# Performance work log

Measured on AMD Instinct MI355X. Metric: run time of the kernel, lower is better.

The kernel has to match this reference:

```python
import jax, jax.numpy as jnp
import numpy as np

B, T, C, H, DH, L, V = 16, 1023, 384, 6, 64, 6, 256
FF = 4 * C
EPS = 1e-5


def _ln(x, g, b):
    mu = x.mean(-1, keepdims=True)
    var = ((x - mu) ** 2).mean(-1, keepdims=True)
    return (x - mu) * jax.lax.rsqrt(var + EPS) * g + b


def setup_inputs() -> dict:
    key = jax.random.key(0)
    ks = jax.random.split(key, 12)
    n = lambda k, shp: jax.random.normal(k, shp, dtype=jnp.float32) * 0.02
    return {
        "x": jax.random.randint(ks[0], (B, T), 0, V),
        "targets": jax.random.randint(ks[1], (B, T), 0, V),
        "tok_emb": n(ks[2], (V, C)),
        "pos_emb": n(ks[3], (T, C)),
        "Wq": n(ks[4], (L, C, C)), "Wk": n(ks[5], (L, C, C)), "Wv": n(ks[6], (L, C, C)),
        "Wo": n(ks[7], (L, C, C)), "bo": jnp.zeros((L, C)),
        "ln1_g": jnp.ones((L, C)), "ln1_b": jnp.zeros((L, C)),
        "ln2_g": jnp.ones((L, C)), "ln2_b": jnp.zeros((L, C)),
        "W1": n(ks[8], (L, C, FF)), "b1": jnp.zeros((L, FF)),
        "W2": n(ks[9], (L, FF, C)), "b2": jnp.zeros((L, C)),
        "lnf_g": jnp.ones((C,)), "lnf_b": jnp.zeros((C,)),
        "Wf": n(ks[10], (C, V)), "bf": jnp.zeros((V,)),
    }


def _forward(x, targets, tok_emb, pos_emb, Wq, Wk, Wv, Wo, bo,
             ln1_g, ln1_b, ln2_g, ln2_b, W1, b1, W2, b2, lnf_g, lnf_b, Wf, bf):
    h = tok_emb[x] + pos_emb[None, :, :]  # [B,T,C]
    tril = jnp.tril(jnp.ones((T, T), bool))

    def heads(z, W):  # [B,T,C] @ [C,C] -> [B,H,T,DH]
        return jnp.einsum('btc,cd->btd', z, W).reshape(B, T, H, DH).transpose(0, 2, 1, 3)

    def layer(h, p):
        wq, wk, wv, wo, bo_, g1, be1, g2, be2, w1, bb1, w2, bb2 = p
        z = _ln(h, g1, be1)
        q, k, v = heads(z, wq), heads(z, wk), heads(z, wv)
        qk = jnp.einsum('bhtd,bhsd->bhts', q, k) * (DH ** -0.5)
        zm = jnp.where(tril, qk, 0.0)
        # faithful to torch: masked_fill_(zeromask == 0, -inf)
        zm = jnp.where(zm == 0.0, -jnp.inf, zm)
        att = jax.nn.softmax(zm, axis=-1)  # dropout = identity (eval)
        o = jnp.einsum('bhts,bhsd->bhtd', att, v).transpose(0, 2, 1, 3).reshape(B, T, C)
        h = h + jnp.einsum('btc,cd->btd', o, wo) + bo_
        z2 = _ln(h, g2, be2)
        ff = jax.nn.relu(jnp.einsum('btc,cf->btf', z2, w1) + bb1)
        h = h + jnp.einsum('btf,fc->btc', ff, w2) + bb2
        return h, None

    params = (Wq, Wk, Wv, Wo, bo, ln1_g, ln1_b, ln2_g, ln2_b, W1, b1, W2, b2)
    h, _ = jax.lax.scan(layer, h, params)
    logits = jnp.einsum('btc,cv->btv', _ln(h, lnf_g, lnf_b), Wf) + bf
    logits2 = logits.reshape(B * T, V)
    logp = jax.nn.log_softmax(logits2, axis=-1)
    loss = -jnp.take_along_axis(logp, targets.reshape(B * T, 1), axis=1).mean()
    return logits2, loss


def reference(x, targets, tok_emb, pos_emb, Wq, Wk, Wv, Wo, bo,
              ln1_g, ln1_b, ln2_g, ln2_b, W1, b1, W2, b2, lnf_g, lnf_b, Wf, bf):
    return _forward(x, targets, tok_emb, pos_emb, Wq, Wk, Wv, Wo, bo,
                    ln1_g, ln1_b, ln2_g, ln2_b, W1, b1, W2, b2, lnf_g, lnf_b, Wf, bf)
```

## Files before the change

kernel.cpp:

```cpp
#include <hip/hip_runtime.h>
#include <hip/hip_bf16.h>
#include <math.h>

#define B_  16
#define T_  1023
#define C_  384
#define H_  6
#define DH_ 64
#define L_  6
#define V_  256
#define FF_ 1536
#define M_  (B_*T_)
#define MP_ 16384
#define EPS_ 1e-5f

typedef __attribute__((ext_vector_type(8))) short bf16x8;
typedef __attribute__((ext_vector_type(4))) short short4v;
typedef __attribute__((ext_vector_type(4))) float f32x4;

__device__ inline short f2bf(float x) {
    union { float f; unsigned u; } c; c.f = x;
    unsigned r = (c.u + 0x7fffu + ((c.u >> 16) & 1u)) >> 16;
    return (short)r;
}

#define GLDS16(g, l) __builtin_amdgcn_global_load_lds(                         \
    (const __attribute__((address_space(1))) void*)(g),                        \
    (__attribute__((address_space(3))) void*)(l), 16, 0, 0)

#define TRRD(dst, va, IMM) asm volatile("ds_read_b64_tr_b16 %0, %1 offset:" IMM \
    : "=v"(dst) : "v"(va))

__global__ void embed_kernel(const int* __restrict__ x, const float* __restrict__ tok,
                             const float* __restrict__ pos, float* __restrict__ h) {
    int i = blockIdx.x * 256 + threadIdx.x;
    if (i >= M_ * C_) return;
    int bt = i / C_;
    int c  = i - bt * C_;
    int t  = bt % T_;
    h[i] = tok[x[bt] * C_ + c] + pos[t * C_ + c];
}

__global__ __launch_bounds__(256) void wconv_kernel(
    const float* __restrict__ Wq, const float* __restrict__ Wk,
    const float* __restrict__ Wv, const float* __restrict__ Wo,
    const float* __restrict__ W1, const float* __restrict__ W2,
    const float* __restrict__ Wf,
    short* __restrict__ qkvt, short* __restrict__ wot, short* __restrict__ w1t,
    short* __restrict__ w2t, short* __restrict__ wft) {
    __shared__ float tile[32][33];
    int t = blockIdx.x;
    const float* src; short* dst; int K, N, tl;
    if (t < 10368) {
        int l = t / 1728, r = t - l * 1728;
        if (r < 432) {
            int which = r / 144; tl = r - which * 144;
            src = (which == 0 ? Wq : which == 1 ? Wk : Wv) + (size_t)l * 384 * 384;
            dst = qkvt + (size_t)l * 1152 * 384 + (size_t)which * 384 * 384;
            K = 384; N = 384;
        } else if (r < 576) {
            tl = r - 432;
            src = Wo + (size_t)l * 384 * 384; dst = wot + (size_t)l * 384 * 384;
            K = 384; N = 384;
        } else if (r < 1152) {
            tl = r - 576;
            src = W1 + (size_t)l * 384 * 1536; dst = w1t + (size_t)l * 1536 * 384;
            K = 384; N = 1536;
        } else {
            tl = r - 1152;
            src = W2 + (size_t)l * 1536 * 384; dst = w2t + (size_t)l * 384 * 1536;
            K = 1536; N = 384;
        }
    } else {
        tl = t - 10368; src = Wf; dst = wft; K = 384; N = 256;
    }
    int ntx = N >> 5;
    int k0 = (tl / ntx) << 5, n0 = (tl % ntx) << 5;
    int rr = threadIdx.x >> 5, cc = threadIdx.x & 31;
#pragma unroll
    for (int p = 0; p < 4; ++p)
        tile[rr + 8 * p][cc] = src[(size_t)(k0 + rr + 8 * p) * N + n0 + cc];
    __syncthreads();
#pragma unroll
    for (int p = 0; p < 4; ++p)
        dst[(size_t)(n0 + rr + 8 * p) * K + k0 + cc] = f2bf(tile[cc][rr + 8 * p]);
}

__global__ __launch_bounds__(512) void qkv_kernel(const float* __restrict__ h,
                                                  const float* __restrict__ lng,
                                                  const float* __restrict__ lnb,
                                                  const short* __restrict__ wt,
                                                  short* __restrict__ outb) {
    __shared__ short Zl[48 * 64 * 8];
    int tid  = threadIdx.x;
    int wave = tid >> 6, lane = tid & 63;
    int g = lane >> 4, r16 = lane & 15;
    int r0 = blockIdx.x * 64;

    const short* wbase = wt + (size_t)(16 * wave + r16) * C_ + 8 * g;
    bf16x8 wf[12];
#pragma unroll
    for (int ks = 0; ks < 12; ++ks) wf[ks] = *(const bf16x8*)(wbase + ks * 32);

    float gv6[6], bv6[6];
#pragma unroll
    for (int i = 0; i < 6; ++i) { gv6[i] = lng[i * 64 + lane]; bv6[i] = lnb[i * 64 + lane]; }

    for (int rr = 0; rr < 8; ++rr) {
        int lrow = 8 * wave + rr;
        const float* rp = h + (size_t)(r0 + lrow) * C_;
        float v[6];
        float s = 0.f, s2 = 0.f;
#pragma unroll
        for (int i = 0; i < 6; ++i) {
            v[i] = rp[i * 64 + lane];
            s += v[i]; s2 += v[i] * v[i];
        }
#pragma unroll
        for (int o = 32; o > 0; o >>= 1) {
            s  += __shfl_xor(s,  o, 64);
            s2 += __shfl_xor(s2, o, 64);
        }
        float mu = s * (1.0f / C_);
        float rs = rsqrtf(s2 * (1.0f / C_) - mu * mu + EPS_);
#pragma unroll
        for (int i = 0; i < 6; ++i) {
            int col = i * 64 + lane;
            Zl[(col >> 3) * 512 + lrow * 8 + (col & 7)] =
                f2bf((v[i] - mu) * rs * gv6[i] + bv6[i]);
        }
    }
    __syncthreads();

    for (int c = 0; c < 9; ++c) {
        f32x4 acc[4];
#pragma unroll
        for (int mj = 0; mj < 4; ++mj) { acc[mj][0]=0.f; acc[mj][1]=0.f; acc[mj][2]=0.f; acc[mj][3]=0.f; }
#pragma unroll
        for (int ks = 0; ks < 12; ++ks) {
#pragma unroll
            for (int mj = 0; mj < 4; ++mj) {
                bf16x8 bz = *(const bf16x8*)(Zl + ((4 * ks + g) * 64 + 16 * mj + r16) * 8);
                acc[mj] = __builtin_amdgcn_mfma_f32_16x16x32_bf16(wf[ks], bz, acc[mj], 0, 0, 0);
            }
        }
        if (c + 1 < 9) {
#pragma unroll
            for (int ks = 0; ks < 12; ++ks)
                wf[ks] = *(const bf16x8*)(wbase + (size_t)(c + 1) * 128 * C_ + ks * 32);
        }
#pragma unroll
        for (int mj = 0; mj < 4; ++mj) {
            short4v ov;
#pragma unroll
            for (int rg = 0; rg < 4; ++rg) ov[rg] = f2bf(acc[mj][rg]);
            *(short4v*)(outb + (size_t)(r0 + 16 * mj + r16) * 1152
                        + 128 * c + 16 * wave + 4 * g) = ov;
        }
    }
}

__global__ __launch_bounds__(512) void wo_ffn_kernel(const short* __restrict__ ob,
                                                     const short* __restrict__ wot_,
                                                     const float* __restrict__ bo,
                                                     float* __restrict__ h,
                                                     const float* __restrict__ lng,
                                                     const float* __restrict__ lnb,
                                                     const short* __restrict__ w1t,
                                                     const short* __restrict__ w2t,
                                                     const float* __restrict__ b1,
                                                     const float* __restrict__ b2) {
    __shared__ short Ol[48 * 64 * 8];
    __shared__ short Zl[48 * 64 * 8];
    __shared__ short Pl[16 * 64 * 8];
    int tid  = threadIdx.x;
    int wave = tid >> 6, lane = tid & 63;
    int g = lane >> 4, r16 = lane & 15;
    int r0 = blockIdx.x * 64;

    {
        const short* go = ob + (size_t)(r0 + lane) * C_ + wave * 8;
        short* lo = Ol + (wave * 64 + lane) * 8;
#pragma unroll
        for (int ro = 0; ro < 6; ++ro) { GLDS16(go, lo); go += 64; lo += 4096; }
    }

    const short* wbase = wot_ + (size_t)(48 * wave + r16) * C_ + 8 * g;
    bf16x8 wf[12];
#pragma unroll
    for (int ks2 = 0; ks2 < 4; ++ks2)
#pragma unroll
        for (int j = 0; j < 3; ++j)
            wf[ks2 * 3 + j] = *(const bf16x8*)(wbase + (size_t)(16 * j) * C_ + 32 * ks2);

    asm volatile("s_waitcnt vmcnt(0)" ::: "memory");
    __builtin_amdgcn_s_barrier();
    asm volatile("" ::: "memory");

    f32x4 acc[4][3];
#pragma unroll
    for (int mi = 0; mi < 4; ++mi)
#pragma unroll
        for (int j = 0; j < 3; ++j) { acc[mi][j][0]=0.f; acc[mi][j][1]=0.f; acc[mi][j][2]=0.f; acc[mi][j][3]=0.f; }

    for (int kc = 0; kc < 3; ++kc) {
#pragma unroll
        for (int ks2 = 0; ks2 < 4; ++ks2) {
            bf16x8 pa[4];
#pragma unroll
            for (int mi = 0; mi < 4; ++mi)
                pa[mi] = *(const bf16x8*)(Ol + ((16 * kc + 4 * ks2 + g) * 64 + 16 * mi + r16) * 8);
#pragma unroll
            for (int j = 0; j < 3; ++j)
#pragma unroll
                for (int mi = 0; mi < 4; ++mi)
                    acc[mi][j] = __builtin_amdgcn_mfma_f32_16x16x32_bf16(pa[mi], wf[ks2 * 3 + j], acc[mi][j], 0, 0, 0);
        }
        if (kc + 1 < 3) {
#pragma unroll
            for (int ks2 = 0; ks2 < 4; ++ks2)
#pragma unroll
                for (int j = 0; j < 3; ++j)
                    wf[ks2 * 3 + j] = *(const bf16x8*)(wbase + (size_t)(16 * j) * C_
                                                       + 128 * (kc + 1) + 32 * ks2);
        }
    }
    __syncthreads();

    const short* w1base = w1t + (size_t)(16 * wave + r16) * C_ + 8 * g;
    const short* w2base = w2t + (size_t)(48 * wave + r16) * FF_ + 8 * g;
    bf16x8 w1f[12];
#pragma unroll
    for (int ks = 0; ks < 12; ++ks)
        w1f[ks] = *(const bf16x8*)(w1base + ks * 32);

    float rsum[4][4], rsq[4][4];
#pragma unroll
    for (int mi = 0; mi < 4; ++mi)
#pragma unroll
        for (int rg = 0; rg < 4; ++rg) { rsum[mi][rg] = 0.f; rsq[mi][rg] = 0.f; }

#pragma unroll
    for (int j = 0; j < 3; ++j) {
        int col = 48 * wave + 16 * j + r16;
        float bj = bo[col];
#pragma unroll
        for (int mi = 0; mi < 4; ++mi) {
#pragma unroll
            for (int rg = 0; rg < 4; ++rg) {
                int row = r0 + 16 * mi + 4 * g + rg;
                float hv = h[(size_t)row * C_ + col] + acc[mi][j][rg] + bj;
                h[(size_t)row * C_ + col] = hv;
                acc[mi][j][rg] = hv;
                rsum[mi][rg] += hv;
                rsq[mi][rg]  += hv * hv;
            }
        }
    }
#pragma unroll
    for (int o = 1; o < 16; o <<= 1) {
#pragma unroll
        for (int mi = 0; mi < 4; ++mi)
#pragma unroll
            for (int rg = 0; rg < 4; ++rg) {
                rsum[mi][rg] += __shfl_xor(rsum[mi][rg], o, 64);
                rsq[mi][rg]  += __shfl_xor(rsq[mi][rg],  o, 64);
            }
    }
    float* St = (float*)Ol;
    if (r16 == 0) {
#pragma unroll
        for (int mi = 0; mi < 4; ++mi)
#pragma unroll
            for (int rg = 0; rg < 4; ++rg) {
                int rr = 16 * mi + 4 * g + rg;
                St[rr * 16 + 2 * wave]     = rsum[mi][rg];
                St[rr * 16 + 2 * wave + 1] = rsq[mi][rg];
            }
    }
    __syncthreads();
    if (tid < 64) {
        float s = 0.f, s2 = 0.f;
#pragma unroll
        for (int w = 0; w < 8; ++w) { s += St[tid * 16 + 2 * w]; s2 += St[tid * 16 + 2 * w + 1]; }
        float mu  = s * (1.0f / C_);
        float var = s2 * (1.0f / C_) - mu * mu;
        St[tid * 16]     = mu;
        St[tid * 16 + 1] = rsqrtf(var + EPS_);
    }
    __syncthreads();
#pragma unroll
    for (int j = 0; j < 3; ++j) {
        int col = 48 * wave + 16 * j + r16;
        float gam = lng[col], bet = lnb[col];
#pragma unroll
        for (int mi = 0; mi < 4; ++mi) {
#pragma unroll
            for (int rg = 0; rg < 4; ++rg) {
                int rr = 16 * mi + 4 * g + rg;
                float mu = St[rr * 16], rs = St[rr * 16 + 1];
                Zl[(col >> 3) * 512 + rr * 8 + (col & 7)] =
                    f2bf((acc[mi][j][rg] - mu) * rs * gam + bet);
            }
        }
    }
    __syncthreads();

    f32x4 acc2[4][3];
#pragma unroll
    for (int mi = 0; mi < 4; ++mi)
#pragma unroll
        for (int j = 0; j < 3; ++j) { acc2[mi][j][0]=0.f; acc2[mi][j][1]=0.f; acc2[mi][j][2]=0.f; acc2[mi][j][3]=0.f; }

    for (int c = 0; c < 12; ++c) {
        bf16x8 w2f[12];
#pragma unroll
        for (int ks2 = 0; ks2 < 4; ++ks2)
#pragma unroll
            for (int j = 0; j < 3; ++j)
                w2f[ks2 * 3 + j] = *(const bf16x8*)(w2base + (size_t)(16 * j) * FF_
                                                    + 128 * c + 32 * ks2);

        f32x4 acc1[4];
#pragma unroll
        for (int mj = 0; mj < 4; ++mj) { acc1[mj][0]=0.f; acc1[mj][1]=0.f; acc1[mj][2]=0.f; acc1[mj][3]=0.f; }
#pragma unroll
        for (int ks = 0; ks < 12; ++ks) {
#pragma unroll
            for (int mj = 0; mj < 4; ++mj) {
                bf16x8 bz = *(const bf16x8*)(Zl + ((4 * ks + g) * 64 + 16 * mj + r16) * 8);
                acc1[mj] = __builtin_amdgcn_mfma_f32_16x16x32_bf16(w1f[ks], bz, acc1[mj], 0, 0, 0);
            }
        }
        f32x4 b1v = *(const f32x4*)(b1 + 128 * c + 16 * wave + 4 * g);
        int oct = 2 * wave + (g >> 1);
#pragma unroll
        for (int mj = 0; mj < 4; ++mj) {
            short4v pv;
#pragma unroll
            for (int rg = 0; rg < 4; ++rg)
                pv[rg] = f2bf(fmaxf(acc1[mj][rg] + b1v[rg], 0.f));
            *(short4v*)(Pl + (oct * 64 + 16 * mj + r16) * 8 + (g & 1) * 4) = pv;
        }
        __syncthreads();

        if (c + 1 < 12) {
#pragma unroll
            for (int ks = 0; ks < 12; ++ks)
                w1f[ks] = *(const bf16x8*)(w1base + (size_t)(c + 1) * 128 * C_ + ks * 32);
        }

#pragma unroll
        for (int ks2 = 0; ks2 < 4; ++ks2) {
            bf16x8 pa[4];
#pragma unroll
            for (int mi = 0; mi < 4; ++mi)
                pa[mi] = *(const bf16x8*)(Pl + ((4 * ks2 + g) * 64 + 16 * mi + r16) * 8);
#pragma unroll
            for (int j = 0; j < 3; ++j) {
#pragma unroll
                for (int mi = 0; mi < 4; ++mi)
                    acc2[mi][j] = __builtin_amdgcn_mfma_f32_16x16x32_bf16(pa[mi], w2f[ks2 * 3 + j], acc2[mi][j], 0, 0, 0);
            }
        }
        __syncthreads();
    }

#pragma unroll
    for (int j = 0; j < 3; ++j) {
        int col = 48 * wave + 16 * j + r16;
        float bj = b2[col];
#pragma unroll
        for (int mi = 0; mi < 4; ++mi) {
#pragma unroll
            for (int rg = 0; rg < 4; ++rg) {
                int row = r0 + 16 * mi + 4 * g + rg;
                h[(size_t)row * C_ + col] += acc2[mi][j][rg] + bj;
            }
        }
    }
}

__global__ __launch_bounds__(512) void final_kernel(const float* __restrict__ h,
                                                    const float* __restrict__ lng,
                                                    const float* __restrict__ lnb,
                                                    const short* __restrict__ wt,
                                                    const float* __restrict__ bf,
                                                    const int* __restrict__ tgt,
                                                    float* __restrict__ logits,
                                                    float* __restrict__ nll) {
    __shared__ short Zl[48 * 64 * 8];
    __shared__ float Lg[64][260];
    int tid  = threadIdx.x;
    int wave = tid >> 6, lane = tid & 63;
    int g = lane >> 4, r16 = lane & 15;
    int r0 = blockIdx.x * 64;

    const short* wbase = wt + (size_t)(16 * wave + r16) * C_ + 8 * g;
    bf16x8 wf[12];
#pragma unroll
    for (int ks = 0; ks < 12; ++ks) wf[ks] = *(const bf16x8*)(wbase + ks * 32);

    float gv6[6], bv6[6];
#pragma unroll
    for (int i = 0; i < 6; ++i) { gv6[i] = lng[i * 64 + lane]; bv6[i] = lnb[i * 64 + lane]; }

    for (int rr = 0; rr < 8; ++rr) {
        int lrow = 8 * wave + rr;
        const float* rp = h + (size_t)(r0 + lrow) * C_;
        float v[6];
        float s = 0.f, s2 = 0.f;
#pragma unroll
        for (int i = 0; i < 6; ++i) {
            v[i] = rp[i * 64 + lane];
            s += v[i]; s2 += v[i] * v[i];
        }
#pragma unroll
        for (int o = 32; o > 0; o >>= 1) {
            s  += __shfl_xor(s,  o, 64);
            s2 += __shfl_xor(s2, o, 64);
        }
        float mu = s * (1.0f / C_);
        float rs = rsqrtf(s2 * (1.0f / C_) - mu * mu + EPS_);
#pragma unroll
        for (int i = 0; i < 6; ++i) {
            int col = i * 64 + lane;
            Zl[(col >> 3) * 512 + lrow * 8 + (col & 7)] =
                f2bf((v[i] - mu) * rs * gv6[i] + bv6[i]);
        }
    }
    __syncthreads();

    for (int c = 0; c < 2; ++c) {
        f32x4 acc[4];
#pragma unroll
        for (int mj = 0; mj < 4; ++mj) { acc[mj][0]=0.f; acc[mj][1]=0.f; acc[mj][2]=0.f; acc[mj][3]=0.f; }
#pragma unroll
        for (int ks = 0; ks < 12; ++ks) {
#pragma unroll
            for (int mj = 0; mj < 4; ++mj) {
                bf16x8 bz = *(const bf16x8*)(Zl + ((4 * ks + g) * 64 + 16 * mj + r16) * 8);
                acc[mj] = __builtin_amdgcn_mfma_f32_16x16x32_bf16(wf[ks], bz, acc[mj], 0, 0, 0);
            }
        }
        if (c + 1 < 2) {
#pragma unroll
            for (int ks = 0; ks < 12; ++ks)
                wf[ks] = *(const bf16x8*)(wbase + (size_t)128 * C_ + ks * 32);
        }
        int colb = 128 * c + 16 * wave + 4 * g;
        f32x4 bv4 = *(const f32x4*)(bf + colb);
#pragma unroll
        for (int mj = 0; mj < 4; ++mj) {
            int lrow = 16 * mj + r16;
            int row  = r0 + lrow;
            f32x4 ov;
#pragma unroll
            for (int rg = 0; rg < 4; ++rg) {
                ov[rg] = acc[mj][rg] + bv4[rg];
                Lg[lrow][colb + rg] = ov[rg];
            }
            if (row < M_) *(f32x4*)(logits + (size_t)row * V_ + colb) = ov;
        }
    }
    __syncthreads();

    for (int rr = 0; rr < 8; ++rr) {
        int lrow = 8 * wave + rr;
        int row  = r0 + lrow;
        float v[4];
        float mx = -INFINITY;
#pragma unroll
        for (int i = 0; i < 4; ++i) {
            v[i] = Lg[lrow][i * 64 + lane];
            mx = fmaxf(mx, v[i]);
        }
#pragma unroll
        for (int o = 32; o > 0; o >>= 1) mx = fmaxf(mx, __shfl_xor(mx, o, 64));
        float s = 0.f;
#pragma unroll
        for (int i = 0; i < 4; ++i) s += expf(v[i] - mx);
#pragma unroll
        for (int o = 32; o > 0; o >>= 1) s += __shfl_xor(s, o, 64);
        if (lane == 0 && row < M_) {
            float lse = mx + logf(s);
            nll[row] = lse - Lg[lrow][tgt[row]];
        }
    }
}

__device__ __forceinline__ void attn_step(int kt, int qg, int g, int r16,
                                          const char* Kb, unsigned ka, unsigned va,
                                          short (*Pw)[40],
                                          bf16x8 qf0, bf16x8 qf1,
                                          f32x4* o_acc, float& m, float& l) {
    f32x4 s0, s1;
    s0[0]=0.f;s0[1]=0.f;s0[2]=0.f;s0[3]=0.f;
    s1[0]=0.f;s1[1]=0.f;s1[2]=0.f;s1[3]=0.f;
    bf16x8 a00 = *(const bf16x8*)(Kb + ka);
    bf16x8 a01 = *(const bf16x8*)(Kb + (ka ^ 64u));
    bf16x8 a10 = *(const bf16x8*)(Kb + ka + 2048u);
    bf16x8 a11 = *(const bf16x8*)(Kb + ((ka + 2048u) ^ 64u));
    s0 = __builtin_amdgcn_mfma_f32_16x16x32_bf16(a00, qf0, s0, 0, 0, 0);
    s0 = __builtin_amdgcn_mfma_f32_16x16x32_bf16(a01, qf1, s0, 0, 0, 0);
    s1 = __builtin_amdgcn_mfma_f32_16x16x32_bf16(a10, qf0, s1, 0, 0, 0);
    s1 = __builtin_amdgcn_mfma_f32_16x16x32_bf16(a11, qf1, s1, 0, 0, 0);

    int kb0 = kt * 32 + 4 * g;
    float sv[8];
#pragma unroll
    for (int r = 0; r < 4; ++r) {
        sv[r]     = (kb0 + r      <= qg) ? s0[r] * 0.125f : -3e38f;
        sv[4 + r] = (kb0 + 16 + r <= qg) ? s1[r] * 0.125f : -3e38f;
    }
    float pmax = sv[0];
#pragma unroll
    for (int i = 1; i < 8; ++i) pmax = fmaxf(pmax, sv[i]);
    pmax = fmaxf(pmax, __shfl_xor(pmax, 16, 64));
    pmax = fmaxf(pmax, __shfl_xor(pmax, 32, 64));
    float mn   = fmaxf(m, pmax);
    float corr = __expf(m - mn);
    float rs = 0.f;
    short pb[8];
#pragma unroll
    for (int i = 0; i < 8; ++i) {
        float p = __expf(sv[i] - mn);
        rs += p;
        pb[i] = f2bf(p);
    }
    rs += __shfl_xor(rs, 16, 64);
    rs += __shfl_xor(rs, 32, 64);
    l = l * corr + rs;
    m = mn;

    short4v t0w, t1w;
    t0w[0]=pb[0]; t0w[1]=pb[1]; t0w[2]=pb[2]; t0w[3]=pb[3];
    t1w[0]=pb[4]; t1w[1]=pb[5]; t1w[2]=pb[6]; t1w[3]=pb[7];
    *(short4v*)&Pw[r16][4 * g]      = t0w;
    *(short4v*)&Pw[r16][16 + 4 * g] = t1w;

    short4v v0, v1, v2, v3, v4, v5, v6, v7;
    TRRD(v0, va, "0");    TRRD(v1, va, "512");
    TRRD(v2, va, "128");  TRRD(v3, va, "640");
    TRRD(v4, va, "256");  TRRD(v5, va, "768");
    TRRD(v6, va, "384");  TRRD(v7, va, "896");

    bf16x8 pB = *(const bf16x8*)&Pw[r16][8 * g];
#pragma unroll
    for (int d = 0; d < 4; ++d) {
        o_acc[d][0] *= corr; o_acc[d][1] *= corr;
        o_acc[d][2] *= corr; o_acc[d][3] *= corr;
    }
    asm volatile("s_waitcnt lgkmcnt(0)" ::: "memory");
    __builtin_amdgcn_sched_barrier(0);

    bf16x8 av0, av1, av2, av3;
#pragma unroll
    for (int i = 0; i < 4; ++i) {
        av0[i] = v0[i]; av0[i + 4] = v1[i];
        av1[i] = v2[i]; av1[i + 4] = v3[i];
        av2[i] = v4[i]; av2[i + 4] = v5[i];
        av3[i] = v6[i]; av3[i + 4] = v7[i];
    }
    o_acc[0] = __builtin_amdgcn_mfma_f32_16x16x32_bf16(av0, pB, o_acc[0], 0, 0, 0);
    o_acc[1] = __builtin_amdgcn_mfma_f32_16x16x32_bf16(av1, pB, o_acc[1], 0, 0, 0);
    o_acc[2] = __builtin_amdgcn_mfma_f32_16x16x32_bf16(av2, pB, o_acc[2], 0, 0, 0);
    o_acc[3] = __builtin_amdgcn_mfma_f32_16x16x32_bf16(av3, pB, o_acc[3], 0, 0, 0);
}

__global__ __launch_bounds__(256) void attn_kernel(const short* __restrict__ qkv,
                                                   short* __restrict__ o) {
    __shared__ short Kl[2][32 * 64];
    __shared__ short Vl[2][32 * 64];
    __shared__ short P_lds[4][16][40];

    int tid  = threadIdx.x;
    int wave = tid >> 6;
    int lane = tid & 63;
    int g    = lane >> 4;
    int r16  = lane & 15;

    int qtA = blockIdx.x;
    int qtB = 15 - qtA;
    int bh = blockIdx.y;
    int b  = bh / H_, hh = bh - b * H_;
    size_t rbase = (size_t)b * T_;
    int qoff = hh * 64;

    int q0A = qtA * 64, q0B = qtB * 64;
    int qgA = q0A + wave * 16 + r16;
    int qgB = q0B + wave * 16 + r16;

    const short* qrA = qkv + (rbase + qgA) * 1152 + qoff;
    const short* qrB = qkv + (rbase + qgB) * 1152 + qoff;
    bf16x8 qfA0 = *(const bf16x8*)(qrA + 8 * g);
    bf16x8 qfA1 = *(const bf16x8*)(qrA + 32 + 8 * g);
    bf16x8 qfB0 = *(const bf16x8*)(qrB + 8 * g);
    bf16x8 qfB1 = *(const bf16x8*)(qrB + 32 + 8 * g);

    int kkey = tid >> 3;
    int koct = (tid & 7) ^ (kkey & 7);
    const short* gk = qkv + (rbase + kkey) * 1152 + qoff + 384 + koct * 8;
    int vkey = 4 * (tid >> 5) + ((tid >> 1) & 3);
    int voct = 2 * ((tid >> 3) & 3) + (tid & 1);
    const short* gv = qkv + (rbase + vkey) * 1152 + qoff + 768 + voct * 8;
    short* lk0 = Kl[0] + tid * 8;
    short* lk1 = Kl[1] + tid * 8;
    short* lv0 = Vl[0] + tid * 8;
    short* lv1 = Vl[1] + tid * 8;

    f32x4 oA[4], oB[4];
#pragma unroll
    for (int d = 0; d < 4; ++d) {
        oA[d][0]=0.f; oA[d][1]=0.f; oA[d][2]=0.f; oA[d][3]=0.f;
        oB[d][0]=0.f; oB[d][1]=0.f; oB[d][2]=0.f; oB[d][3]=0.f;
    }
    float mA = -3e38f, lA = 0.f, mB = -3e38f, lB = 0.f;

    const char* Kb0 = (const char*)Kl[0];
    const char* Kb1 = (const char*)Kl[1];
    unsigned ka = (unsigned)(r16 * 128 + ((g ^ (r16 & 7)) << 4));
    unsigned va0 = (unsigned)(size_t)(__attribute__((address_space(3))) short*)Vl[0]
                 + 1024u * (unsigned)g + 8u * (unsigned)r16;
    unsigned va1 = va0 + 4096u;

    int ktA_hi = (q0A + wave * 16 + 15) >> 5;
    int ktB_hi = (q0B + wave * 16 + 15) >> 5;
    int nkt = 2 * (qtB + 1);

    GLDS16(gk, lk0);
    GLDS16(gv, lv0);
    gk += 32 * 1152; gv += 32 * 1152;
    asm volatile("s_waitcnt vmcnt(0)" ::: "memory");
    __builtin_amdgcn_s_barrier();
    asm volatile("" ::: "memory");

    for (int kt = 0; kt < nkt; ++kt) {
        int cur = kt & 1;
        if (kt + 1 < nkt) {
            GLDS16(gk, cur ? lk0 : lk1);
            GLDS16(gv, cur ? lv0 : lv1);
            gk += 32 * 1152; gv += 32 * 1152;
        }
        const char* Kb = cur ? Kb1 : Kb0;
        unsigned va = cur ? va1 : va0;

        if (kt <= ktB_hi)
            attn_step(kt, qgB, g, r16, Kb, ka, va, P_lds[wave], qfB0, qfB1, oB, mB, lB);
        if (kt <= ktA_hi)
            attn_step(kt, qgA, g, r16, Kb, ka, va, P_lds[wave], qfA0, qfA1, oA, mA, lA);

        asm volatile("s_waitcnt vmcnt(0)" ::: "memory");
        __builtin_amdgcn_s_barrier();
        asm volatile("" ::: "memory");
    }

    {
        float inv = (lA > 0.f) ? 1.f / lA : 0.f;
        short* orow = o + (rbase + qgA) * C_ + qoff;
#pragma unroll
        for (int d = 0; d < 4; ++d) {
            short4v ov;
#pragma unroll
            for (int r = 0; r < 4; ++r) ov[r] = f2bf(oA[d][r] * inv);
            *(short4v*)(orow + 16 * d + 4 * g) = ov;
        }
    }
    if (qgB < T_) {
        float inv = (lB > 0.f) ? 1.f / lB : 0.f;
        short* orow = o + (rbase + qgB) * C_ + qoff;
#pragma unroll
        for (int d = 0; d < 4; ++d) {
            short4v ov;
#pragma unroll
            for (int r = 0; r < 4; ++r) ov[r] = f2bf(oB[d][r] * inv);
            *(short4v*)(orow + 16 * d + 4 * g) = ov;
        }
    }
}

__global__ __launch_bounds__(256) void loss_kernel(const float* __restrict__ nll,
                                                   float* __restrict__ loss) {
    __shared__ float sm[256];
    float s = 0.f;
    for (int i = threadIdx.x; i < M_; i += 256) s += nll[i];
    sm[threadIdx.x] = s;
    __syncthreads();
    for (int o = 128; o > 0; o >>= 1) {
        if (threadIdx.x < o) sm[threadIdx.x] += sm[threadIdx.x + o];
        __syncthreads();
    }
    if (threadIdx.x == 0) *loss = sm[0] * (1.0f / M_);
}

extern "C" void kernel_launch(void* const* d_in, const int* in_sizes, int n_in,
                              void* d_out, int out_size, void* d_ws, size_t ws_size,
                              hipStream_t stream) {
    const int*   x       = (const int*)d_in[0];
    const int*   targets = (const int*)d_in[1];
    const float* tok_emb = (const float*)d_in[2];
    const float* pos_emb = (const float*)d_in[3];
    const float* Wq      = (const float*)d_in[4];
    const float* Wk      = (const float*)d_in[5];
    const float* Wv      = (const float*)d_in[6];
    const float* Wo      = (const float*)d_in[7];
    const float* bo      = (const float*)d_in[8];
    const float* ln1_g   = (const float*)d_in[9];
    const float* ln1_b   = (const float*)d_in[10];
    const float* ln2_g   = (const float*)d_in[11];
    const float* ln2_b   = (const float*)d_in[12];
    const float* W1      = (const float*)d_in[13];
    const float* b1      = (const float*)d_in[14];
    const float* W2      = (const float*)d_in[15];
    const float* b2      = (const float*)d_in[16];
    const float* lnf_g   = (const float*)d_in[17];
    const float* lnf_b   = (const float*)d_in[18];
    const float* Wf      = (const float*)d_in[19];
    const float* bf      = (const float*)d_in[20];

    float* logits = (float*)d_out;
    float* loss   = logits + (size_t)M_ * V_;

    float* h    = (float*)d_ws;
    short* z    = (short*)(h + (size_t)MP_ * C_);
    short* big  = z + (size_t)MP_ * C_;
    short* ob   = big + (size_t)MP_ * FF_;
    short* qkvt = ob + (size_t)MP_ * C_;
    short* wot  = qkvt + (size_t)L_ * 1152 * 384;
    short* w1t  = wot + (size_t)L_ * 384 * 384;
    short* w2t  = w1t + (size_t)L_ * 1536 * 384;
    short* wft  = w2t + (size_t)L_ * 1536 * 384;
    float* nll  = (float*)(wft + (size_t)256 * 384);

    wconv_kernel<<<10464, 256, 0, stream>>>(Wq, Wk, Wv, Wo, W1, W2, Wf,
                                            qkvt, wot, w1t, w2t, wft);
    embed_kernel<<<(M_ * C_ + 255) / 256, 256, 0, stream>>>(x, tok_emb, pos_emb, h);

    for (int l = 0; l < L_; ++l) {
        qkv_kernel<<<MP_ / 64, 512, 0, stream>>>(
            h, ln1_g + l * C_, ln1_b + l * C_,
            qkvt + (size_t)l * 1152 * 384, big);
        attn_kernel<<<dim3(8, B_ * H_), 256, 0, stream>>>(big, ob);
        wo_ffn_kernel<<<MP_ / 64, 512, 0, stream>>>(
            ob, wot + (size_t)l * 384 * 384, bo + l * C_, h,
            ln2_g + l * C_, ln2_b + l * C_,
            w1t + (size_t)l * 1536 * 384, w2t + (size_t)l * 384 * 1536,
            b1 + l * FF_, b2 + l * C_);
        ffn_dummy:;
    }

    final_kernel<<<MP_ / 64, 512, 0, stream>>>(
        h, lnf_g, lnf_b, wft, bf, targets, logits, nll);
    loss_kernel<<<1, 256, 0, stream>>>(nll, loss);
}
```

Before: 1.132 ms.

## Fuse next layer's LN1 and QKV projection into wo_ffn kernel epilogue

After the FFN residual update, the wo_ffn kernel now computes row statistics from the fresh h values held in registers, applies the next layer's LN1, stages the result in shared memory, and runs the QKV projection for the next layer. Only the first layer keeps a standalone qkv launch. This removes five kernel launches and a round trip of h through global memory per layer. In exchange it adds register and shared-memory pressure to an already large kernel, which may lower occupancy.

```diff
diff --git a/kernel.cpp b/kernel.cpp
--- a/kernel.cpp
+++ b/kernel.cpp
@@ -169,7 +169,12 @@
                                                      const short* __restrict__ w1t,
                                                      const short* __restrict__ w2t,
                                                      const float* __restrict__ b1,
-                                                     const float* __restrict__ b2) {
+                                                     const float* __restrict__ b2,
+                                                     int next_qkv,
+                                                     const float* __restrict__ n1g,
+                                                     const float* __restrict__ n1b,
+                                                     const short* __restrict__ nqw,
+                                                     short* __restrict__ big) {
     __shared__ short Ol[48 * 64 * 8];
     __shared__ short Zl[48 * 64 * 8];
     __shared__ short Pl[16 * 64 * 8];
@@ -367,6 +372,11 @@
     }
 
 #pragma unroll
+    for (int mi = 0; mi < 4; ++mi)
+#pragma unroll
+        for (int rg = 0; rg < 4; ++rg) { rsum[mi][rg] = 0.f; rsq[mi][rg] = 0.f; }
+
+#pragma unroll
     for (int j = 0; j < 3; ++j) {
         int col = 48 * wave + 16 * j + r16;
         float bj = b2[col];
@@ -375,8 +385,95 @@
 #pragma unroll
             for (int rg = 0; rg < 4; ++rg) {
                 int row = r0 + 16 * mi + 4 * g + rg;
-                h[(size_t)row * C_ + col] += acc2[mi][j][rg] + bj;
-            }
+                float hv = h[(size_t)row * C_ + col] + acc2[mi][j][rg] + bj;
+                h[(size_t)row * C_ + col] = hv;
+                acc2[mi][j][rg] = hv;
+                rsum[mi][rg] += hv;
+                rsq[mi][rg]  += hv * hv;
+            }
+        }
+    }
+
+    if (!next_qkv) return;
+
+    const short* nwbase = nqw + (size_t)(16 * wave + r16) * C_ + 8 * g;
+#pragma unroll
+    for (int ks = 0; ks < 12; ++ks)
+        w1f[ks] = *(const bf16x8*)(nwbase + ks * 32);
+
+#pragma unroll
+    for (int o = 1; o < 16; o <<= 1) {
+#pragma unroll
+        for (int mi = 0; mi < 4; ++mi)
+#pragma unroll
+            for (int rg = 0; rg < 4; ++rg) {
+                rsum[mi][rg] += __shfl_xor(rsum[mi][rg], o, 64);
+                rsq[mi][rg]  += __shfl_xor(rsq[mi][rg],  o, 64);
+            }
+    }
+    __syncthreads();
+    if (r16 == 0) {
+#pragma unroll
+        for (int mi = 0; mi < 4; ++mi)
+#pragma unroll
+            for (int rg = 0; rg < 4; ++rg) {
+                int rr = 16 * mi + 4 * g + rg;
+                St[rr * 16 + 2 * wave]     = rsum[mi][rg];
+                St[rr * 16 + 2 * wave + 1] = rsq[mi][rg];
+            }
+    }
+    __syncthreads();
+    if (tid < 64) {
+        float s = 0.f, s2 = 0.f;
+#pragma unroll
+        for (int w = 0; w < 8; ++w) { s += St[tid * 16 + 2 * w]; s2 += St[tid * 16 + 2 * w + 1]; }
+        float mu  = s * (1.0f / C_);
+        float var = s2 * (1.0f / C_) - mu * mu;
+        St[tid * 16]     = mu;
+        St[tid * 16 + 1] = rsqrtf(var + EPS_);
+    }
+    __syncthreads();
+#pragma unroll
+    for (int j = 0; j < 3; ++j) {
+        int col = 48 * wave + 16 * j + r16;
+        float gam = n1g[col], bet = n1b[col];
+#pragma unroll
+        for (int mi = 0; mi < 4; ++mi) {
+#pragma unroll
+            for (int rg = 0; rg < 4; ++rg) {
+                int rr = 16 * mi + 4 * g + rg;
+                float mu = St[rr * 16], rs = St[rr * 16 + 1];
+                Zl[(col >> 3) * 512 + rr * 8 + (col & 7)] =
+                    f2bf((acc2[mi][j][rg] - mu) * rs * gam + bet);
+            }
+        }
+    }
+    __syncthreads();
+
+    for (int c = 0; c < 9; ++c) {
+        f32x4 qacc[4];
+#pragma unroll
+        for (int mj = 0; mj < 4; ++mj) { qacc[mj][0]=0.f; qacc[mj][1]=0.f; qacc[mj][2]=0.f; qacc[mj][3]=0.f; }
+#pragma unroll
+        for (int ks = 0; ks < 12; ++ks) {
+#pragma unroll
+            for (int mj = 0; mj < 4; ++mj) {
+                bf16x8 bz = *(const bf16x8*)(Zl + ((4 * ks + g) * 64 + 16 * mj + r16) * 8);
+                qacc[mj] = __builtin_amdgcn_mfma_f32_16x16x32_bf16(w1f[ks], bz, qacc[mj], 0, 0, 0);
+            }
+        }
+        if (c + 1 < 9) {
+#pragma unroll
+            for (int ks = 0; ks < 12; ++ks)
+                w1f[ks] = *(const bf16x8*)(nwbase + (size_t)(c + 1) * 128 * C_ + ks * 32);
+        }
+#pragma unroll
+        for (int mj = 0; mj < 4; ++mj) {
+            short4v ov;
+#pragma unroll
+            for (int rg = 0; rg < 4; ++rg) ov[rg] = f2bf(qacc[mj][rg]);
+            *(short4v*)(big + (size_t)(r0 + 16 * mj + r16) * 1152
+                        + 128 * c + 16 * wave + 4 * g) = ov;
         }
     }
 }
@@ -736,17 +833,22 @@
                                             qkvt, wot, w1t, w2t, wft);
     embed_kernel<<<(M_ * C_ + 255) / 256, 256, 0, stream>>>(x, tok_emb, pos_emb, h);
 
+    qkv_kernel<<<MP_ / 64, 512, 0, stream>>>(
+        h, ln1_g, ln1_b, qkvt, big);
+
     for (int l = 0; l < L_; ++l) {
-        qkv_kernel<<<MP_ / 64, 512, 0, stream>>>(
-            h, ln1_g + l * C_, ln1_b + l * C_,
-            qkvt + (size_t)l * 1152 * 384, big);
         attn_kernel<<<dim3(8, B_ * H_), 256, 0, stream>>>(big, ob);
+        int nq = (l + 1 < L_) ? 1 : 0;
         wo_ffn_kernel<<<MP_ / 64, 512, 0, stream>>>(
             ob, wot + (size_t)l * 384 * 384, bo + l * C_, h,
             ln2_g + l * C_, ln2_b + l * C_,
             w1t + (size_t)l * 1536 * 384, w2t + (size_t)l * 384 * 1536,
-            b1 + l * FF_, b2 + l * C_);
-        ffn_dummy:;
+            b1 + l * FF_, b2 + l * C_,
+            nq,
+            ln1_g + (l + 1 < L_ ? (l + 1) * C_ : 0),
+            ln1_b + (l + 1 < L_ ? (l + 1) * C_ : 0),
+            qkvt + (size_t)(l + 1 < L_ ? (l + 1) : 0) * 1152 * 384,
+            big);
     }
 
     final_kernel<<<MP_ / 64, 512, 0, stream>>>(
```

Measured after the change: 1.149 ms. About the same (+1.5%).
